# Kernel tuning notes

Measured on AMD Instinct MI355X. Metric: run time of the kernel, lower is better.

The kernel has to match this reference:

```python
import jax, jax.numpy as jnp
import numpy as np
import math

SR = 96000.0
FRAME = 2048          # FRAME_SIZE
NB = 16               # N_BIQUADS
B, F = 16, 128        # batch, n_frames
N = F * FRAME         # n_samples (divisible by FRAME)

GAIN_RANGE = (-24.0, 24.0)
BROADBAND = (-60.0, 0.0)
Q_RANGE = (0.5, 16.0)
HPF_R = (20.0, 500.0)
LPF_R = (5000.0, 20000.0)
SHELF_R = (50.0, 16000.0)
PEAK_R = (100.0, 15000.0)


def _denorm_freq(n, r):
    lo, hi = math.log(r[0]), math.log(r[1])
    return jnp.exp(lo + n * (hi - lo))


def _denorm_gain(n, r):
    return r[0] + n * (r[1] - r[0])


def _denorm_q(n):
    lo, hi = math.log(Q_RANGE[0]), math.log(Q_RANGE[1])
    return jnp.exp(lo + n * (hi - lo))


def _norm(b0, b1, b2, a0, a1, a2):
    return b0 / a0, b1 / a0, b2 / a0, a1 / a0, a2 / a0


def _hp(fc, Q):
    w0 = 2 * math.pi * fc / SR
    al = jnp.sin(w0) / (2 * Q)
    c = jnp.cos(w0)
    return _norm((1 + c) / 2, -(1 + c), (1 + c) / 2, 1 + al, -2 * c, 1 - al)


def _lp(fc, Q):
    w0 = 2 * math.pi * fc / SR
    al = jnp.sin(w0) / (2 * Q)
    c = jnp.cos(w0)
    return _norm((1 - c) / 2, 1 - c, (1 - c) / 2, 1 + al, -2 * c, 1 - al)


def _peak(fc, g_db, Q):
    A = jnp.power(10.0, g_db / 40.0)
    w0 = 2 * math.pi * fc / SR
    al = jnp.sin(w0) / (2 * Q)
    c = jnp.cos(w0)
    return _norm(1 + al * A, -2 * c, 1 - al * A, 1 + al / A, -2 * c, 1 - al / A)


def _lowshelf(fc, g_db, Q):
    A = jnp.power(10.0, g_db / 40.0)
    w0 = 2 * math.pi * fc / SR
    al = jnp.sin(w0) / (2 * Q)
    c = jnp.cos(w0)
    sA = jnp.sqrt(A)
    b0 = A * (A + 1 - (A - 1) * c + 2 * sA * al)
    b1 = 2 * A * (A - 1 - (A + 1) * c)
    b2 = A * (A + 1 - (A - 1) * c - 2 * sA * al)
    a0 = A + 1 + (A - 1) * c + 2 * sA * al
    a1 = -2 * (A - 1 + (A + 1) * c)
    a2 = A + 1 + (A - 1) * c - 2 * sA * al
    return _norm(b0, b1, b2, a0, a1, a2)


def _highshelf(fc, g_db, Q):
    A = jnp.power(10.0, g_db / 40.0)
    w0 = 2 * math.pi * fc / SR
    al = jnp.sin(w0) / (2 * Q)
    c = jnp.cos(w0)
    sA = jnp.sqrt(A)
    b0 = A * (A + 1 + (A - 1) * c + 2 * sA * al)
    b1 = -2 * A * (A - 1 + (A + 1) * c)
    b2 = A * (A + 1 + (A - 1) * c - 2 * sA * al)
    a0 = A + 1 - (A - 1) * c + 2 * sA * al
    a1 = 2 * (A - 1 - (A + 1) * c)
    a2 = A + 1 - (A - 1) * c - 2 * sA * al
    return _norm(b0, b1, b2, a0, a1, a2)


def _forward(audio, params):
    b, n = audio.shape
    f = n // FRAME
    fp = params.shape[2]
    # per-audio-frame parameter index: min(frame_idx, n_frames_params-1)
    idx = jnp.minimum(jnp.arange(f), fp - 1)
    p = params[:, :, idx]                       # (B, 50, F)
    bq = p[:, : NB * 3, :].reshape(b, NB, 3, f)  # (B, 16, 3, F)
    in_g = jnp.power(10.0, _denorm_gain(p[:, -2, :], BROADBAND) / 20.0)   # (B,F)
    out_g = jnp.power(10.0, _denorm_gain(p[:, -1, :], BROADBAND) / 20.0)  # (B,F)

    x = audio.reshape(b, f, FRAME) * in_g[:, :, None]

    # per-stage normalized coefficients, each (B, F)
    coefs = []
    for i in range(NB):
        fn, gn, qn = bq[:, i, 0], bq[:, i, 1], bq[:, i, 2]
        Q = _denorm_q(qn)
        if i == 0:                      # BIQUAD_HPF
            c = _hp(_denorm_freq(fn, HPF_R), Q)
        elif i == NB - 1:               # BIQUAD_LPF
            c = _lp(_denorm_freq(fn, LPF_R), Q)
        elif i == 1:                    # BIQUAD_LOW_SHELF
            c = _lowshelf(_denorm_freq(fn, SHELF_R), _denorm_gain(gn, GAIN_RANGE), Q)
        elif i == NB - 2:               # BIQUAD_HIGH_SHELF
            c = _highshelf(_denorm_freq(fn, SHELF_R), _denorm_gain(gn, GAIN_RANGE), Q)
        else:                           # peaking EQ
            c = _peak(_denorm_freq(fn, PEAK_R), _denorm_gain(gn, GAIN_RANGE), Q)
        coefs.append(jnp.stack(c))      # (5, B, F)
    C = jnp.stack(coefs).reshape(NB, 5, b * f)  # (16, 5, B*F)

    # each (batch, frame) lane filters independently with zero initial state
    xt = x.reshape(b * f, FRAME).T              # (T, B*F)

    def step(s, v):
        # s: (16, 2, B*F) DF2T states; v: (B*F,) cascade input
        new_s = []
        for i in range(NB):
            b0, b1, b2, a1, a2 = C[i, 0], C[i, 1], C[i, 2], C[i, 3], C[i, 4]
            y = b0 * v + s[i, 0]
            s1 = b1 * v - a1 * y + s[i, 1]
            s2 = b2 * v - a2 * y
            new_s.append(jnp.stack([s1, s2]))
            v = y
        return jnp.stack(new_s), v

    s0 = jnp.zeros((NB, 2, b * f), dtype=audio.dtype)
    _, ys = jax.lax.scan(step, s0, xt)          # (T, B*F)

    y = ys.T.reshape(b, f, FRAME) * out_g[:, :, None]
    return y.reshape(b, n)


def setup_inputs() -> dict:
    key = jax.random.key(0)
    k1, k2 = jax.random.split(key)
    audio = jax.random.normal(k1, (B, N), dtype=jnp.float32)
    params = jax.random.uniform(k2, (B, 50, F), dtype=jnp.float32)
    return {"audio": audio, "params": params}


def reference(audio, params):
    return _forward(audio, params)
```

## Files before the change

kernel.cpp:

```cpp
#include <hip/hip_runtime.h>
#include <math.h>

namespace {

constexpr int kNB    = 16;
constexpr int kFrame = 2048;
constexpr int kHalf  = 16;

typedef float f32x2 __attribute__((ext_vector_type(2)));

__device__ inline f32x2 pk_fma(f32x2 a, f32x2 b, f32x2 c) {
    f32x2 d;
    asm("v_pk_fma_f32 %0, %1, %2, %3" : "=v"(d) : "v"(a), "v"(b), "v"(c));
    return d;
}
__device__ inline f32x2 pk_mul(f32x2 a, f32x2 b) {
    f32x2 d;
    asm("v_pk_mul_f32 %0, %1, %2" : "=v"(d) : "v"(a), "v"(b));
    return d;
}
__device__ inline f32x2 pk_add(f32x2 a, f32x2 b) {
    f32x2 d;
    asm("v_pk_add_f32 %0, %1, %2" : "=v"(d) : "v"(a), "v"(b));
    return d;
}

template <int CTRL>
__device__ inline float dpp_f(float v) {
    return __int_as_float(
        __builtin_amdgcn_update_dpp(0, __float_as_int(v), CTRL, 0xF, 0xF, true));
}

template <int CTRL>
__device__ inline void ks_level(float& v0, float& v1, const float4 M, const float na1) {
    const float t0 = dpp_f<CTRL>(v0);
    const float t1 = dpp_f<CTRL>(v1);
    const float w  = fmaf(na1, t0, t1);
    v0 = fmaf(M.x, w,  fmaf(M.y, t0, v0));
    v1 = fmaf(M.z, t0, fmaf(M.y, t1, v1));
}

__global__ __launch_bounds__(64)
void biquad_chain_kernel(const float* __restrict__ audio,
                         const float* __restrict__ params,
                         float* __restrict__ out)
{
    __shared__ float4 sK[kNB][2];
    __shared__ float4 powT[kNB][33];

    const int lane = threadIdx.x & 63;
    const int ch   = blockIdx.x;
    const int bb   = ch >> 7;
    const int ff   = ch & 127;

    const float* pb = params + (size_t)bb * (50 * 128) + ff;

    {
        const int band = lane & 15;
        const int part = lane >> 4;
        const float fn = pb[(band * 3 + 0) * 128];
        const float gn = pb[(band * 3 + 1) * 128];
        const float qn = pb[(band * 3 + 2) * 128];

        const bool isHP = (band == 0), isLP = (band == kNB - 1);
        const bool isShelf = (band == 1) || (band == kNB - 2);
        const float flo = isHP ? 2.995732274f
                        : isLP ? 8.517193191f
                        : isShelf ? 3.912023005f
                        : 4.605170186f;
        const float fsp = isHP ? 3.218875825f
                        : isLP ? 1.386294361f
                        : isShelf ? 5.768320996f
                        : 5.010635294f;

        const float Q  = __expf(fmaf(qn, 3.465735903f, -0.6931471806f));
        const float fc = __expf(fmaf(fn, fsp, flo));
        const float hw = fc * 3.272492349e-5f;
        const float x2 = hw * hw;
        const float sh = hw * fmaf(x2, fmaf(x2, fmaf(x2, -1.984126984e-4f,
                                   8.333333333e-3f), -0.1666666667f), 1.0f);
        const float chh = sqrtf(fmaf(-sh, sh, 1.0f));
        const float sw  = 2.0f * sh * chh;
        const float ver = 2.0f * sh * sh;
        const float alq = sw / (Q + Q);
        const float gdb = (isHP || isLP) ? 0.f : fmaf(gn, 48.f, -24.f);
        const float A   = __expf(gdb * 0.05756462732f);
        const float sA  = sqrtf(A);
        const float ge  = isHP ? fmaf(pb[48 * 128], 60.f, -60.f) * 0.1151292546f
                        : isLP ? fmaf(pb[49 * 128], 60.f, -60.f) * 0.1151292546f
                        : 0.f;
        const float gm  = __expf(ge);

        float b0, b1, b2, a0, a1, a2;
        if (isHP) {
            b0 = 1.0f - 0.5f * ver; b1 = ver - 2.0f; b2 = b0;
            a0 = 1.0f + alq; a1 = 2.0f * ver - 2.0f; a2 = 1.0f - alq;
        } else if (isLP) {
            b0 = 0.5f * ver; b1 = ver; b2 = b0;
            a0 = 1.0f + alq; a1 = 2.0f * ver - 2.0f; a2 = 1.0f - alq;
        } else if (band == 1) {
            const float t = 2.0f * sA * alq;
            const float u = (A - 1.0f) * ver;
            const float w = (A + 1.0f) * ver;
            b0 = A * (2.0f + u + t);
            b1 = A * (2.0f * w - 4.0f);
            b2 = A * (2.0f + u - t);
            a0 = 2.0f * A - u + t;
            a1 = 2.0f * w - 4.0f * A;
            a2 = 2.0f * A - u - t;
        } else if (band == kNB - 2) {
            const float t = 2.0f * sA * alq;
            const float u = (A - 1.0f) * ver;
            const float w = (A + 1.0f) * ver;
            b0 = A * (2.0f * A - u + t);
            b1 = -2.0f * A * (2.0f * A - w);
            b2 = A * (2.0f * A - u - t);
            a0 = 2.0f + u + t;
            a1 = 2.0f * w - 4.0f;
            a2 = 2.0f + u - t;
        } else {
            const float alA  = alq * A;
            const float aloA = alq / A;
            b0 = 1.0f + alA; b1 = 2.0f * ver - 2.0f; b2 = 1.0f - alA;
            a0 = 1.0f + aloA; a1 = b1; a2 = 1.0f - aloA;
        }
        const float inv  = 1.0f / a0;
        const float binv = inv * gm;
        b0 *= binv; b1 *= binv; b2 *= binv;
        a1 *= inv; a2 *= inv;

        const double a1d = (double)a1, a2d = (double)a2;
        double alc = 1.0, bec = 0.0;
        double al16 = 0, be16 = 0, al32 = 0, be32 = 0;
        double al256 = 0, be256 = 0, al512 = 0, be512 = 0;
        #pragma unroll
        for (int k = 1; k <= 9; ++k) {
            const double a_ = alc, b_ = bec;
            alc = a_ * (2.0 * b_ - a1d * a_);
            bec = b_ * b_ - a2d * (a_ * a_);
            if (k == 4) { al16 = alc; be16 = bec; }
            if (k == 5) { al32 = alc; be32 = bec; }
            if (k == 8) { al256 = alc; be256 = bec; }
            if (k == 9) { al512 = alc; be512 = bec; }
        }
        auto cmp = [&](double alx, double bex, double aly, double bey,
                       double& alo, double& beo) {
            const double p = alx * aly;
            alo = alx * bey + bex * aly - a1d * p;
            beo = bex * bey - a2d * p;
        };

        double Sa, Sb;
        if (part == 0)      { Sa = al32; Sb = be32; }
        else if (part == 1) { cmp(al256, be256, al32, be32, Sa, Sb); }
        else if (part == 2) { cmp(al512, be512, al32, be32, Sa, Sb); }
        else { double ta, tb; cmp(al512, be512, al256, be256, ta, tb);
               cmp(ta, tb, al32, be32, Sa, Sb); }

        #pragma unroll
        for (int j = 0; j < 8; ++j) {
            powT[band][8 * part + j] =
                float4{(float)Sa, (float)Sb, (float)(-a2d * Sa), 0.f};
            double na, nb;
            cmp(Sa, Sb, al32, be32, na, nb);
            Sa = na; Sb = nb;
        }
        if (part == 0) {
            sK[band][0] = float4{b0, b1, b2, -a1};
            sK[band][1] = float4{-a2, (float)al16, (float)be16,
                                 (float)(-a2d * al16)};
        }
    }
    __syncthreads();

    f32x2 X[kHalf];
    {
        const float4* ap = reinterpret_cast<const float4*>(
            audio + (size_t)ch * kFrame + lane * 32);
        #pragma unroll
        for (int k = 0; k < 4; ++k) {
            const float4 va = ap[k];
            const float4 vb = ap[k + 4];
            X[4 * k + 0] = f32x2{va.x, vb.x};
            X[4 * k + 1] = f32x2{va.y, vb.y};
            X[4 * k + 2] = f32x2{va.z, vb.z};
            X[4 * k + 3] = f32x2{va.w, vb.w};
        }
    }

    float4 k0 = sK[0][0], k1 = sK[0][1];
    f32x2 b0p  = {k0.x, k0.x}, b1p = {k0.y, k0.y}, b2p = {k0.z, k0.z};
    f32x2 na1p = {k0.w, k0.w}, na2p = {k1.x, k1.x};

    f32x2 s1 = {0.f, 0.f}, s2 = {0.f, 0.f};
    #pragma unroll
    for (int t = 0; t < kHalf; ++t) {
        const f32x2 xv = X[t];
        const f32x2 y  = pk_fma(b0p, xv, s1);
        const f32x2 tm = pk_fma(b1p, xv, s2);
        s2 = pk_fma(na2p, y, pk_mul(b2p, xv));
        s1 = pk_fma(na1p, y, tm);
        X[t] = y;
    }

    for (int band = 0; band < kNB; ++band) {
        const float na1 = na1p.x;
        const float al16 = k1.y, be16 = k1.z, ga16 = k1.w;

        const float4 P1 = powT[band][0];
        const float4 P2 = powT[band][1];
        const float4 P4 = powT[band][3];
        const float4 P8 = powT[band][7];
        const float4 Pme = powT[band][lane & 15];
        const float4 Qme = powT[band][lane & 31];

        const float wf = fmaf(na1, s1.x, s2.x);
        const float d0 = fmaf(al16, wf, fmaf(be16, s1.x, s1.y));
        const float d1 = fmaf(ga16, s1.x, fmaf(be16, s2.x, s2.y));

        float v0 = dpp_f<0x138>(d0);
        float v1 = dpp_f<0x138>(d1);
        ks_level<0x111>(v0, v1, P1, na1);
        ks_level<0x112>(v0, v1, P2, na1);
        ks_level<0x114>(v0, v1, P4, na1);
        ks_level<0x118>(v0, v1, P8, na1);
        {
            float t0 = dpp_f<0x142>(v0);
            float t1 = dpp_f<0x142>(v1);
            const bool g = (lane & 16) != 0;
            t0 = g ? t0 : 0.f;
            t1 = g ? t1 : 0.f;
            const float w = fmaf(na1, t0, t1);
            v0 = fmaf(Pme.x, w,  fmaf(Pme.y, t0, v0));
            v1 = fmaf(Pme.z, t0, fmaf(Pme.y, t1, v1));
        }
        {
            float t0 = dpp_f<0x143>(v0);
            float t1 = dpp_f<0x143>(v1);
            const bool g = lane >= 32;
            t0 = g ? t0 : 0.f;
            t1 = g ? t1 : 0.f;
            const float w = fmaf(na1, t0, t1);
            v0 = fmaf(Qme.x, w,  fmaf(Qme.y, t0, v0));
            v1 = fmaf(Qme.z, t0, fmaf(Qme.y, t1, v1));
        }

        const float wr  = fmaf(na1, v0, v1);
        const float uB0 = fmaf(al16, wr, fmaf(be16, v0, s1.x));
        const float uB1 = fmaf(ga16, v0, fmaf(be16, v1, s2.x));
        f32x2 cw0 = {v0, uB0}, cw1 = {v1, uB1};

        if (band == kNB - 1) {
            #pragma unroll
            for (int t = 0; t < kHalf; ++t) {
                const f32x2 cc = cw0;
                X[t] = pk_add(X[t], cc);
                cw0 = pk_fma(na1p, cc, cw1);
                cw1 = pk_mul(na2p, cc);
            }
            break;
        }

        const float4 nk0 = sK[band + 1][0];
        const float4 nk1 = sK[band + 1][1];
        const f32x2 nb0p  = {nk0.x, nk0.x}, nb1p = {nk0.y, nk0.y};
        const f32x2 nb2p  = {nk0.z, nk0.z};
        const f32x2 nna1p = {nk0.w, nk0.w}, nna2p = {nk1.x, nk1.x};

        s1 = f32x2{0.f, 0.f}; s2 = f32x2{0.f, 0.f};
        #pragma unroll
        for (int t = 0; t < kHalf; ++t) {
            const f32x2 cc = cw0;
            cw0 = pk_fma(na1p, cc, cw1);
            cw1 = pk_mul(na2p, cc);
            const f32x2 xv = pk_add(X[t], cc);
            const f32x2 y  = pk_fma(nb0p, xv, s1);
            const f32x2 tm = pk_fma(nb1p, xv, s2);
            s2 = pk_fma(nna2p, y, pk_mul(nb2p, xv));
            s1 = pk_fma(nna1p, y, tm);
            X[t] = y;
        }

        k0 = nk0; k1 = nk1;
        b0p = nb0p; b1p = nb1p; b2p = nb2p; na1p = nna1p; na2p = nna2p;
    }

    {
        float4* op = reinterpret_cast<float4*>(out + (size_t)ch * kFrame + lane * 32);
        #pragma unroll
        for (int k = 0; k < 4; ++k) {
            op[k]     = float4{X[4 * k + 0].x, X[4 * k + 1].x, X[4 * k + 2].x, X[4 * k + 3].x};
            op[k + 4] = float4{X[4 * k + 0].y, X[4 * k + 1].y, X[4 * k + 2].y, X[4 * k + 3].y};
        }
    }
}

}

extern "C" void kernel_launch(void* const* d_in, const int* in_sizes, int n_in,
                              void* d_out, int out_size, void* d_ws, size_t ws_size,
                              hipStream_t stream)
{
    (void)d_ws; (void)ws_size; (void)n_in; (void)in_sizes;
    const float* audio  = (const float*)d_in[0];
    const float* params = (const float*)d_in[1];
    float* outp = (float*)d_out;

    const int channels = out_size / kFrame;
    hipLaunchKernelGGL(biquad_chain_kernel, dim3(channels), dim3(64), 0, stream,
                       audio, params, outp);
}
```

Baseline: 28.00 us.

## Unfuse correction and next-band filter passes; hoist audio load before coefficient setup

Moves the global audio load ahead of the coefficient and power-table computation so memory latency can overlap with the setup math. The per-band structure is split back into three steps: a zero-state filter pass, a scan, then a separate homogeneous correction pass, instead of fusing the correction into the next band's filter pass. This simplifies the loop body and register live ranges but adds an extra sweep over the 16 register pairs per band.

```diff
diff --git a/kernel.cpp b/kernel.cpp
--- a/kernel.cpp
+++ b/kernel.cpp
@@ -54,6 +54,21 @@
     const int ff   = ch & 127;
 
     const float* pb = params + (size_t)bb * (50 * 128) + ff;
+
+    f32x2 X[kHalf];
+    {
+        const float4* ap = reinterpret_cast<const float4*>(
+            audio + (size_t)ch * kFrame + lane * 32);
+        #pragma unroll
+        for (int k = 0; k < 4; ++k) {
+            const float4 va = ap[k];
+            const float4 vb = ap[k + 4];
+            X[4 * k + 0] = f32x2{va.x, vb.x};
+            X[4 * k + 1] = f32x2{va.y, vb.y};
+            X[4 * k + 2] = f32x2{va.z, vb.z};
+            X[4 * k + 3] = f32x2{va.w, vb.w};
+        }
+    }
 
     {
         const int band = lane & 15;
@@ -173,46 +188,31 @@
     }
     __syncthreads();
 
-    f32x2 X[kHalf];
-    {
-        const float4* ap = reinterpret_cast<const float4*>(
-            audio + (size_t)ch * kFrame + lane * 32);
-        #pragma unroll
-        for (int k = 0; k < 4; ++k) {
-            const float4 va = ap[k];
-            const float4 vb = ap[k + 4];
-            X[4 * k + 0] = f32x2{va.x, vb.x};
-            X[4 * k + 1] = f32x2{va.y, vb.y};
-            X[4 * k + 2] = f32x2{va.z, vb.z};
-            X[4 * k + 3] = f32x2{va.w, vb.w};
-        }
-    }
-
-    float4 k0 = sK[0][0], k1 = sK[0][1];
-    f32x2 b0p  = {k0.x, k0.x}, b1p = {k0.y, k0.y}, b2p = {k0.z, k0.z};
-    f32x2 na1p = {k0.w, k0.w}, na2p = {k1.x, k1.x};
-
-    f32x2 s1 = {0.f, 0.f}, s2 = {0.f, 0.f};
-    #pragma unroll
-    for (int t = 0; t < kHalf; ++t) {
-        const f32x2 xv = X[t];
-        const f32x2 y  = pk_fma(b0p, xv, s1);
-        const f32x2 tm = pk_fma(b1p, xv, s2);
-        s2 = pk_fma(na2p, y, pk_mul(b2p, xv));
-        s1 = pk_fma(na1p, y, tm);
-        X[t] = y;
-    }
-
     for (int band = 0; band < kNB; ++band) {
-        const float na1 = na1p.x;
-        const float al16 = k1.y, be16 = k1.z, ga16 = k1.w;
-
+        const float4 k0 = sK[band][0];
+        const float4 k1 = sK[band][1];
         const float4 P1 = powT[band][0];
         const float4 P2 = powT[band][1];
         const float4 P4 = powT[band][3];
         const float4 P8 = powT[band][7];
         const float4 Pme = powT[band][lane & 15];
         const float4 Qme = powT[band][lane & 31];
+
+        const float b0 = k0.x, b1 = k0.y, b2 = k0.z, na1 = k0.w;
+        const float na2 = k1.x, al16 = k1.y, be16 = k1.z, ga16 = k1.w;
+        const f32x2 b0p  = {b0, b0},  b1p = {b1, b1}, b2p = {b2, b2};
+        const f32x2 na1p = {na1, na1}, na2p = {na2, na2};
+
+        f32x2 s1 = {0.f, 0.f}, s2 = {0.f, 0.f};
+        #pragma unroll
+        for (int t = 0; t < kHalf; ++t) {
+            const f32x2 xv = X[t];
+            const f32x2 y  = pk_fma(b0p, xv, s1);
+            const f32x2 tm = pk_fma(b1p, xv, s2);
+            s2 = pk_fma(na2p, y, pk_mul(b2p, xv));
+            s1 = pk_fma(na1p, y, tm);
+            X[t] = y;
+        }
 
         const float wf = fmaf(na1, s1.x, s2.x);
         const float d0 = fmaf(al16, wf, fmaf(be16, s1.x, s1.y));
@@ -248,41 +248,15 @@
         const float wr  = fmaf(na1, v0, v1);
         const float uB0 = fmaf(al16, wr, fmaf(be16, v0, s1.x));
         const float uB1 = fmaf(ga16, v0, fmaf(be16, v1, s2.x));
-        f32x2 cw0 = {v0, uB0}, cw1 = {v1, uB1};
-
-        if (band == kNB - 1) {
-            #pragma unroll
-            for (int t = 0; t < kHalf; ++t) {
-                const f32x2 cc = cw0;
-                X[t] = pk_add(X[t], cc);
-                cw0 = pk_fma(na1p, cc, cw1);
-                cw1 = pk_mul(na2p, cc);
-            }
-            break;
-        }
-
-        const float4 nk0 = sK[band + 1][0];
-        const float4 nk1 = sK[band + 1][1];
-        const f32x2 nb0p  = {nk0.x, nk0.x}, nb1p = {nk0.y, nk0.y};
-        const f32x2 nb2p  = {nk0.z, nk0.z};
-        const f32x2 nna1p = {nk0.w, nk0.w}, nna2p = {nk1.x, nk1.x};
-
-        s1 = f32x2{0.f, 0.f}; s2 = f32x2{0.f, 0.f};
+
+        f32x2 w0 = {v0, uB0}, w1 = {v1, uB1};
         #pragma unroll
         for (int t = 0; t < kHalf; ++t) {
-            const f32x2 cc = cw0;
-            cw0 = pk_fma(na1p, cc, cw1);
-            cw1 = pk_mul(na2p, cc);
-            const f32x2 xv = pk_add(X[t], cc);
-            const f32x2 y  = pk_fma(nb0p, xv, s1);
-            const f32x2 tm = pk_fma(nb1p, xv, s2);
-            s2 = pk_fma(nna2p, y, pk_mul(nb2p, xv));
-            s1 = pk_fma(nna1p, y, tm);
-            X[t] = y;
-        }
-
-        k0 = nk0; k1 = nk1;
-        b0p = nb0p; b1p = nb1p; b2p = nb2p; na1p = nna1p; na2p = nna2p;
+            const f32x2 c = w0;
+            X[t] = pk_add(X[t], c);
+            w0 = pk_fma(na1p, c, w1);
+            w1 = pk_mul(na2p, c);
+        }
     }
 
     {
```

New measurement: 27.05 us. 1.03x faster.
